# Kernel optimization log

Hardware: AMD Instinct MI355X
Metric: run time of the kernel (lower is better)

Reference implementation:

```python
import jax, jax.numpy as jnp
import numpy as np

B, N, F_IN, F_OUT, H = 4, 2048, 128, 256, 4
HD = F_OUT // H


def setup_inputs() -> dict:
    key = jax.random.key(0)
    k1, k2, k3, k4, k5 = jax.random.split(key, 5)
    x = jax.random.normal(k1, (B, N, F_IN), dtype=jnp.float32)
    adj = jax.random.randint(k2, (B, N, N), 0, 2, dtype=jnp.int32)
    # xavier-ish scaled params
    W = jax.random.normal(k3, (F_OUT, F_IN), dtype=jnp.float32) * float(np.sqrt(2.0 / (F_IN + F_OUT)))
    a_l = jax.random.normal(k4, (H, HD), dtype=jnp.float32) * float(np.sqrt(2.0 / (H * HD + 1)))
    a_r = jax.random.normal(k5, (H, HD), dtype=jnp.float32) * float(np.sqrt(2.0 / (H * HD + 1)))
    return {"x": x, "adj": adj, "W": W, "a_l": a_l, "a_r": a_r}


def reference(x, adj, W, a_l, a_r):
    Bb, Nn, _ = x.shape
    h = jnp.einsum('bnf,of->bno', x, W).reshape(Bb, Nn, H, HD)   # [B,N,H,HD]
    e_l = jnp.einsum('bnhd,hd->bnh', h, a_l)                      # [B,N,H]
    e_r = jnp.einsum('bnhd,hd->bnh', h, a_r)                      # [B,N,H]
    e = e_l[:, :, None, :] + e_r[:, None, :, :]                   # [B,N(i),N(j),H]
    e = jax.nn.leaky_relu(e, negative_slope=0.2)
    e = jnp.where(adj[..., None] == 0, -jnp.inf, e)
    alpha = jax.nn.softmax(e, axis=2)                             # softmax over neighbors j
    out = jnp.einsum('bijh,bjhd->bihd', alpha, h)                 # [B,N,H,HD]
    return out.reshape(Bb, Nn, F_OUT)
```

## Files before the change

kernel.cpp:

```cpp
#include <hip/hip_runtime.h>
#include <stdint.h>

#define BB 4
#define NN 2048
#define F_IN 128
#define F_OUT 256
#define NH 4
#define HD 64

typedef float f32x4 __attribute__((ext_vector_type(4)));
typedef float f32x2 __attribute__((ext_vector_type(2)));
typedef short s16x8 __attribute__((ext_vector_type(8)));
typedef int i32x4 __attribute__((ext_vector_type(4)));
typedef unsigned long long u64;
typedef unsigned short u16;

#define LOG2E 1.4426950408889634f

__device__ __forceinline__ u16 f32_to_bf16_rtn(float f) {
    union { float f; uint32_t u; } v; v.f = f;
    uint32_t u = v.u;
    u += 0x7fffu + ((u >> 16) & 1u);
    return (u16)(u >> 16);
}

__device__ __forceinline__ float exp2_fast(float x) {
#if __has_builtin(__builtin_amdgcn_exp2f)
    return __builtin_amdgcn_exp2f(x);
#else
    return exp2f(x);
#endif
}

__device__ __forceinline__ int sbfe1(uint32_t v, int k) {
#if __has_builtin(__builtin_amdgcn_sbfe)
    return __builtin_amdgcn_sbfe((int)v, k, 1);
#else
    return ((int32_t)(v << (31 - k))) >> 31;
#endif
}

__global__ __launch_bounds__(256) void k01(
    const int* __restrict__ adj, const float* __restrict__ x,
    const float* __restrict__ W, const float* __restrict__ a_l,
    const float* __restrict__ a_r, u64* __restrict__ abits,
    u16* __restrict__ hB, float* __restrict__ el, f32x2* __restrict__ er12)
{
    const int t = threadIdx.x;

    __shared__ __align__(16) float xs[16][F_IN];
    __shared__ __align__(16) float redl[4 * 64 * 20];
    __shared__ __align__(16) float redr[4 * 64 * 20];

    if (blockIdx.x >= 512) {
        const int wid = ((blockIdx.x - 512) << 2) | (t >> 6);
        const int lane = t & 63;
        const int* rowp = adj + (size_t)wid * NN;
        u64 mym = 0;
#pragma unroll 8
        for (int jt = 0; jt < 32; ++jt) {
            int v = rowp[jt * 64 + lane];
            u64 m = __ballot(v != 0);
            if (lane == jt) mym = m;
        }
        if (lane < 32) abits[(size_t)wid * 32 + lane] = mym;
        return;
    }

    const int b = blockIdx.x >> 7;
    const int n0 = (blockIdx.x & 127) * 16;

    {
        const f32x4* src = (const f32x4*)(x + ((size_t)b * NN + n0) * F_IN);
        f32x4* dst = (f32x4*)&xs[0][0];
        dst[t] = src[t];
        dst[t + 256] = src[t + 256];
    }
    __syncthreads();

    float acc[16];
#pragma unroll
    for (int n = 0; n < 16; ++n) acc[n] = 0.f;

    const float* wrow = W + (size_t)t * F_IN;
#pragma unroll 2
    for (int k0 = 0; k0 < F_IN; k0 += 8) {
        f32x4 w0 = *(const f32x4*)(wrow + k0);
        f32x4 w1 = *(const f32x4*)(wrow + k0 + 4);
#pragma unroll
        for (int n = 0; n < 16; ++n) {
            f32x4 xa = *(const f32x4*)&xs[n][k0];
            f32x4 xb = *(const f32x4*)&xs[n][k0 + 4];
            float s = acc[n];
            s = fmaf(xa[0], w0[0], s); s = fmaf(xa[1], w0[1], s);
            s = fmaf(xa[2], w0[2], s); s = fmaf(xa[3], w0[3], s);
            s = fmaf(xb[0], w1[0], s); s = fmaf(xb[1], w1[1], s);
            s = fmaf(xb[2], w1[2], s); s = fmaf(xb[3], w1[3], s);
            acc[n] = s;
        }
    }

    const int w = t >> 6, lane = t & 63;
    const float al = a_l[t];
    const float ar = a_r[t];
    {
        float* rl = &redl[((size_t)w * 64 + lane) * 20];
        float* rr = &redr[((size_t)w * 64 + lane) * 20];
#pragma unroll
        for (int q = 0; q < 4; ++q) {
            f32x4 vl, vr;
#pragma unroll
            for (int e = 0; e < 4; ++e) {
                vl[e] = acc[q * 4 + e] * al;
                vr[e] = acc[q * 4 + e] * ar;
            }
            *(f32x4*)(rl + q * 4) = vl;
            *(f32x4*)(rr + q * 4) = vr;
        }
    }
    __syncthreads();
    {
        const int n_ = lane & 15, og = lane >> 4;
        float sl = 0.f, sr = 0.f;
#pragma unroll
        for (int oo = 0; oo < 16; ++oo) {
            const int o = og + 4 * oo;
            sl += redl[((size_t)w * 64 + o) * 20 + n_];
            sr += redr[((size_t)w * 64 + o) * 20 + n_];
        }
        sl += __shfl_xor(sl, 16, 64); sl += __shfl_xor(sl, 32, 64);
        sr += __shfl_xor(sr, 16, 64); sr += __shfl_xor(sr, 32, 64);
        if (lane < 16) {
            el[((size_t)b * NH + w) * NN + n0 + lane] = sl * LOG2E;
            float sre = sr * LOG2E;
            f32x2 v2; v2[0] = exp2_fast(sre); v2[1] = exp2_fast(0.2f * sre);
            er12[((size_t)b * NH + w) * NN + n0 + lane] = v2;
        }
    }

    const int dcol = t & 15, cb = (t >> 4) & 3;
    const int jt32 = n0 >> 5;
    const int lb = dcol + ((n0 >> 3) & 2) * 16;
    u16* hb = hB + ((((size_t)b * 64 + jt32) * 4 + w) * 4 + cb) * 512 + (size_t)lb * 8;
    s16x8 pk0, pk1;
#pragma unroll
    for (int n = 0; n < 8; ++n) pk0[n] = (short)f32_to_bf16_rtn(acc[n]);
#pragma unroll
    for (int n = 0; n < 8; ++n) pk1[n] = (short)f32_to_bf16_rtn(acc[n + 8]);
    *(s16x8*)hb         = pk0;
    *(s16x8*)(hb + 128) = pk1;
}

__global__ __launch_bounds__(256, 3) void k2_attn(
    const uint32_t* __restrict__ abits32, const u16* __restrict__ hB,
    const float* __restrict__ el, const f32x2* __restrict__ er12,
    float* __restrict__ out)
{
    const int t = threadIdx.x;
    const int jq = t >> 6, l = t & 63;
    int bid = blockIdx.x;
    bid = (bid & 7) * 128 + (bid >> 3);
    const int b = bid >> 8;
    const int w = (bid >> 6) & 3;
    const int i0 = (bid & 63) * 32;
    const int r = l & 15;
    const int kb = l >> 4;
    const int ks = kb * 8;
    const int irow0 = i0 + r, irow1 = irow0 + 16;

    const u16* hbp = hB + ((((size_t)b * 64 + jq * 16) * 4 + w) * 4) * 512 + (size_t)l * 8;
    const f32x2* erp = er12 + ((size_t)b * NH + w) * NN + jq * 512 + ks;
    const i32x4* m0p4 = (const i32x4*)(abits32 + ((size_t)b * NN + irow0) * 64 + jq * 16);
    const i32x4* m1p4 = (const i32x4*)(abits32 + ((size_t)b * NN + irow1) * 64 + jq * 16);

    const float eli0 = el[((size_t)b * NH + w) * NN + irow0];
    const float eli1 = el[((size_t)b * NH + w) * NN + irow1];
    const float E1i0 = exp2_fast(eli0), E2i0 = exp2_fast(0.2f * eli0);
    const float E1i1 = exp2_fast(eli1), E2i1 = exp2_fast(0.2f * eli1);

    f32x4 a00 = {0.f,0.f,0.f,0.f}, a01 = a00, a02 = a00, a03 = a00, as0 = a00;
    f32x4 a10 = a00, a11 = a00, a12 = a00, a13 = a00, as1 = a00;
    s16x8 ones;
#pragma unroll
    for (int k = 0; k < 8; ++k) ones[k] = (short)0x3F80;

    i32x4 mg0c = m0p4[0], mg1c = m1p4[0];
    s16x8 b0c = *(const s16x8*)(hbp + 0 * 512);
    s16x8 b1c = *(const s16x8*)(hbp + 1 * 512);
    s16x8 b2c = *(const s16x8*)(hbp + 2 * 512);
    s16x8 b3c = *(const s16x8*)(hbp + 3 * 512);
    f32x4 v0c = *(const f32x4*)(erp);
    f32x4 v1c = *(const f32x4*)(erp + 2);
    f32x4 v2c = *(const f32x4*)(erp + 4);
    f32x4 v3c = *(const f32x4*)(erp + 6);
    __builtin_amdgcn_sched_barrier(0);

#define MFMA_BF16 __builtin_amdgcn_mfma_f32_16x16x32_bf16
#define BODY(IT, S, PF)                                                       \
    {                                                                         \
        s16x8 b0n, b1n, b2n, b3n;                                             \
        f32x4 v0n, v1n, v2n, v3n;                                             \
        if (PF) {                        \
            const u16* hp_ = hbp + (size_t)((IT) + 1) * 8192;                 \
            b0n = *(const s16x8*)(hp_ + 0 * 512);                             \
            b1n = *(const s16x8*)(hp_ + 1 * 512);                             \
            b2n = *(const s16x8*)(hp_ + 2 * 512);                             \
            b3n = *(const s16x8*)(hp_ + 3 * 512);                             \
            const f32x2* ep_ = erp + ((IT) + 1) * 32;                         \
            v0n = *(const f32x4*)(ep_);                                       \
            v1n = *(const f32x4*)(ep_ + 2);                                   \
            v2n = *(const f32x4*)(ep_ + 4);                                   \
            v3n = *(const f32x4*)(ep_ + 6);                                   \
        }                                                                     \
        __builtin_amdgcn_sched_barrier(0);                                    \
        uint32_t w2a = ((uint32_t)mg0c[S]) >> ks;                             \
        uint32_t w2b = ((uint32_t)mg1c[S]) >> ks;                             \
        uint32_t pua[8], pub[8];                                              \
        _Pragma("unroll")                                                     \
        for (int k = 0; k < 8; ++k) {                                         \
            f32x4 vv = (k < 2) ? v0c : ((k < 4) ? v1c : ((k < 6) ? v2c : v3c)); \
            float ej1 = vv[(k & 1) * 2];                                      \
            float ej2 = vv[(k & 1) * 2 + 1];                                  \
            float t0 = E1i0 * ej1, m0 = E2i0 * ej2;                           \
            float t1 = E1i1 * ej1, m1 = E2i1 * ej2;                           \
            float p0 = (t0 >= 1.0f) ? t0 : m0;                                \
            float p1 = (t1 >= 1.0f) ? t1 : m1;                                \
            union { float f; uint32_t u; } c0, c1; c0.f = p0; c1.f = p1;      \
            pua[k] = c0.u & (uint32_t)sbfe1(w2a, k);                          \
            pub[k] = c1.u & (uint32_t)sbfe1(w2b, k);                          \
        }                                                                     \
        union { s16x8 v; uint32_t u[4]; } afa, afb;                           \
        afa.u[0] = __builtin_amdgcn_perm(pua[1], pua[0], 0x07060302);         \
        afa.u[1] = __builtin_amdgcn_perm(pua[3], pua[2], 0x07060302);         \
        afa.u[2] = __builtin_amdgcn_perm(pua[5], pua[4], 0x07060302);         \
        afa.u[3] = __builtin_amdgcn_perm(pua[7], pua[6], 0x07060302);         \
        afb.u[0] = __builtin_amdgcn_perm(pub[1], pub[0], 0x07060302);         \
        afb.u[1] = __builtin_amdgcn_perm(pub[3], pub[2], 0x07060302);         \
        afb.u[2] = __builtin_amdgcn_perm(pub[5], pub[4], 0x07060302);         \
        afb.u[3] = __builtin_amdgcn_perm(pub[7], pub[6], 0x07060302);         \
        a00 = MFMA_BF16(afa.v, b0c, a00, 0, 0, 0);                            \
        a01 = MFMA_BF16(afa.v, b1c, a01, 0, 0, 0);                            \
        a02 = MFMA_BF16(afa.v, b2c, a02, 0, 0, 0);                            \
        a03 = MFMA_BF16(afa.v, b3c, a03, 0, 0, 0);                            \
        as0 = MFMA_BF16(afa.v, ones, as0, 0, 0, 0);                           \
        a10 = MFMA_BF16(afb.v, b0c, a10, 0, 0, 0);                            \
        a11 = MFMA_BF16(afb.v, b1c, a11, 0, 0, 0);                            \
        a12 = MFMA_BF16(afb.v, b2c, a12, 0, 0, 0);                            \
        a13 = MFMA_BF16(afb.v, b3c, a13, 0, 0, 0);                            \
        as1 = MFMA_BF16(afb.v, ones, as1, 0, 0, 0);                           \
        if (PF) { b0c = b0n; b1c = b1n; b2c = b2n; b3c = b3n;                 \
                  v0c = v0n; v1c = v1n; v2c = v2n; v3c = v3n; }               \
    }

    for (int g = 0; g < 3; ++g) {
        i32x4 mg0n = m0p4[g + 1];
        i32x4 mg1n = m1p4[g + 1];
        __builtin_amdgcn_sched_barrier(0);
#pragma unroll
        for (int s = 0; s < 4; ++s) {
            const int it = g * 4 + s;
            BODY(it, s, 1);
        }
        mg0c = mg0n; mg1c = mg1n;
    }
#pragma unroll
    for (int s = 0; s < 4; ++s) {
        const int it = 12 + s;
        if (s < 3) { BODY(it, s, 1); } else { BODY(it, s, 0); }
    }

    __shared__ __align__(16) float racc[3 * 64 * 44];
    if (jq > 0) {
        float* p = &racc[((jq - 1) * 64 + l) * 44];
        *(f32x4*)(p +  0) = a00; *(f32x4*)(p +  4) = a01;
        *(f32x4*)(p +  8) = a02; *(f32x4*)(p + 12) = a03;
        *(f32x4*)(p + 16) = as0;
        *(f32x4*)(p + 20) = a10; *(f32x4*)(p + 24) = a11;
        *(f32x4*)(p + 28) = a12; *(f32x4*)(p + 32) = a13;
        *(f32x4*)(p + 36) = as1;
    }
    __syncthreads();
    if (jq == 0) {
#pragma unroll
        for (int s = 0; s < 3; ++s) {
            const float* p = &racc[(s * 64 + l) * 44];
            a00 += *(const f32x4*)(p +  0); a01 += *(const f32x4*)(p +  4);
            a02 += *(const f32x4*)(p +  8); a03 += *(const f32x4*)(p + 12);
            as0 += *(const f32x4*)(p + 16);
            a10 += *(const f32x4*)(p + 20); a11 += *(const f32x4*)(p + 24);
            a12 += *(const f32x4*)(p + 28); a13 += *(const f32x4*)(p + 32);
            as1 += *(const f32x4*)(p + 36);
        }

        float* op = out + ((size_t)b * NN + i0) * F_OUT + w * HD;
#pragma unroll
        for (int q = 0; q < 4; ++q) {
            const int row0 = kb * 4 + q;
            float inv0 = 1.0f / as0[q];
            op[(size_t)row0 * F_OUT +  0 + r] = a00[q] * inv0;
            op[(size_t)row0 * F_OUT + 16 + r] = a01[q] * inv0;
            op[(size_t)row0 * F_OUT + 32 + r] = a02[q] * inv0;
            op[(size_t)row0 * F_OUT + 48 + r] = a03[q] * inv0;
            const int row1 = 16 + kb * 4 + q;
            float inv1 = 1.0f / as1[q];
            op[(size_t)row1 * F_OUT +  0 + r] = a10[q] * inv1;
            op[(size_t)row1 * F_OUT + 16 + r] = a11[q] * inv1;
            op[(size_t)row1 * F_OUT + 32 + r] = a12[q] * inv1;
            op[(size_t)row1 * F_OUT + 48 + r] = a13[q] * inv1;
        }
    }
}

extern "C" void kernel_launch(void* const* d_in, const int* in_sizes, int n_in,
                              void* d_out, int out_size, void* d_ws, size_t ws_size,
                              hipStream_t stream) {
    const float* x   = (const float*)d_in[0];
    const int*   adj = (const int*)d_in[1];
    const float* W   = (const float*)d_in[2];
    const float* a_l = (const float*)d_in[3];
    const float* a_r = (const float*)d_in[4];
    float* out = (float*)d_out;

    char* ws = (char*)d_ws;
    u16*   hB    = (u16*)ws;
    u64*   abits = (u64*)(ws + (size_t)BB * F_OUT * NN * 2);
    float* el    = (float*)(ws + (size_t)BB * F_OUT * NN * 2 + (size_t)BB * NN * 32 * 8);
    f32x2* er12  = (f32x2*)(el + (size_t)BB * NH * NN);

    k01<<<512 + BB * NN / 4, 256, 0, stream>>>(adj, x, W, a_l, a_r, abits, hB, el, er12);
    k2_attn<<<BB * NH * (NN / 32), 256, 0, stream>>>((const uint32_t*)abits, hB, el, er12, out);
}
```

Measured before the change: 48.01 us.

## Stage er and mask tiles in LDS, raise k2 occupancy, shrink k01 shared memory

In the attention kernel, the per-head er12 vector and the 32-row adjacency bitmask tile are loaded cooperatively into shared memory once per block. The inner loop then reads them from LDS instead of issuing per-iteration global prefetches, which frees registers and allows the launch bound to rise from 3 to 4 blocks per CU. The reduction buffer is aliased onto the same shared memory after an extra barrier. In k01, the two reduction buffers are merged into one that is used twice with added barriers to cut LDS use, and the adjacency bit-packing loop batches eight loads before its ballots. The trade-off is more LDS traffic and extra syncs in exchange for fewer global loads and higher occupancy.

```diff
diff --git a/kernel.cpp b/kernel.cpp
--- a/kernel.cpp
+++ b/kernel.cpp
@@ -49,19 +49,22 @@
     const int t = threadIdx.x;
 
     __shared__ __align__(16) float xs[16][F_IN];
-    __shared__ __align__(16) float redl[4 * 64 * 20];
-    __shared__ __align__(16) float redr[4 * 64 * 20];
+    __shared__ __align__(16) float red[4 * 64 * 20];
 
     if (blockIdx.x >= 512) {
         const int wid = ((blockIdx.x - 512) << 2) | (t >> 6);
         const int lane = t & 63;
         const int* rowp = adj + (size_t)wid * NN;
         u64 mym = 0;
-#pragma unroll 8
-        for (int jt = 0; jt < 32; ++jt) {
-            int v = rowp[jt * 64 + lane];
-            u64 m = __ballot(v != 0);
-            if (lane == jt) mym = m;
+        for (int g = 0; g < 4; ++g) {
+            int v[8];
+#pragma unroll
+            for (int u = 0; u < 8; ++u) v[u] = rowp[(g * 8 + u) * 64 + lane];
+#pragma unroll
+            for (int u = 0; u < 8; ++u) {
+                u64 m = __ballot(v[u] != 0);
+                if (lane == g * 8 + u) mym = m;
+            }
         }
         if (lane < 32) abits[(size_t)wid * 32 + lane] = mym;
         return;
@@ -103,39 +106,52 @@
     const int w = t >> 6, lane = t & 63;
     const float al = a_l[t];
     const float ar = a_r[t];
-    {
-        float* rl = &redl[((size_t)w * 64 + lane) * 20];
-        float* rr = &redr[((size_t)w * 64 + lane) * 20];
+    const int n_ = lane & 15, og = lane >> 4;
+    float sl, sr;
+    {
+        float* rp = &red[((size_t)w * 64 + lane) * 20];
 #pragma unroll
         for (int q = 0; q < 4; ++q) {
-            f32x4 vl, vr;
-#pragma unroll
-            for (int e = 0; e < 4; ++e) {
-                vl[e] = acc[q * 4 + e] * al;
-                vr[e] = acc[q * 4 + e] * ar;
-            }
-            *(f32x4*)(rl + q * 4) = vl;
-            *(f32x4*)(rr + q * 4) = vr;
-        }
-    }
-    __syncthreads();
-    {
-        const int n_ = lane & 15, og = lane >> 4;
-        float sl = 0.f, sr = 0.f;
-#pragma unroll
-        for (int oo = 0; oo < 16; ++oo) {
-            const int o = og + 4 * oo;
-            sl += redl[((size_t)w * 64 + o) * 20 + n_];
-            sr += redr[((size_t)w * 64 + o) * 20 + n_];
-        }
-        sl += __shfl_xor(sl, 16, 64); sl += __shfl_xor(sl, 32, 64);
-        sr += __shfl_xor(sr, 16, 64); sr += __shfl_xor(sr, 32, 64);
-        if (lane < 16) {
-            el[((size_t)b * NH + w) * NN + n0 + lane] = sl * LOG2E;
-            float sre = sr * LOG2E;
-            f32x2 v2; v2[0] = exp2_fast(sre); v2[1] = exp2_fast(0.2f * sre);
-            er12[((size_t)b * NH + w) * NN + n0 + lane] = v2;
-        }
+            f32x4 v;
+#pragma unroll
+            for (int e = 0; e < 4; ++e) v[e] = acc[q * 4 + e] * al;
+            *(f32x4*)(rp + q * 4) = v;
+        }
+    }
+    __syncthreads();
+    {
+        float s = 0.f;
+#pragma unroll
+        for (int oo = 0; oo < 16; ++oo)
+            s += red[((size_t)w * 64 + og + 4 * oo) * 20 + n_];
+        s += __shfl_xor(s, 16, 64); s += __shfl_xor(s, 32, 64);
+        sl = s;
+    }
+    __syncthreads();
+    {
+        float* rp = &red[((size_t)w * 64 + lane) * 20];
+#pragma unroll
+        for (int q = 0; q < 4; ++q) {
+            f32x4 v;
+#pragma unroll
+            for (int e = 0; e < 4; ++e) v[e] = acc[q * 4 + e] * ar;
+            *(f32x4*)(rp + q * 4) = v;
+        }
+    }
+    __syncthreads();
+    {
+        float s = 0.f;
+#pragma unroll
+        for (int oo = 0; oo < 16; ++oo)
+            s += red[((size_t)w * 64 + og + 4 * oo) * 20 + n_];
+        s += __shfl_xor(s, 16, 64); s += __shfl_xor(s, 32, 64);
+        sr = s;
+    }
+    if (lane < 16) {
+        el[((size_t)b * NH + w) * NN + n0 + lane] = sl * LOG2E;
+        float sre = sr * LOG2E;
+        f32x2 v2; v2[0] = exp2_fast(sre); v2[1] = exp2_fast(0.2f * sre);
+        er12[((size_t)b * NH + w) * NN + n0 + lane] = v2;
     }
 
     const int dcol = t & 15, cb = (t >> 4) & 3;
@@ -151,11 +167,18 @@
     *(s16x8*)(hb + 128) = pk1;
 }
 
-__global__ __launch_bounds__(256, 3) void k2_attn(
+#define MSTRIDE 68
+
+__global__ __launch_bounds__(256, 4) void k2_attn(
     const uint32_t* __restrict__ abits32, const u16* __restrict__ hB,
     const float* __restrict__ el, const f32x2* __restrict__ er12,
     float* __restrict__ out)
 {
+    __shared__ __align__(16) char smem[33792];
+    float*    er_lds   = (float*)smem;
+    uint32_t* mask_lds = (uint32_t*)(smem + 16384);
+    float*    racc     = (float*)smem;
+
     const int t = threadIdx.x;
     const int jq = t >> 6, l = t & 63;
     int bid = blockIdx.x;
@@ -168,11 +191,20 @@
     const int ks = kb * 8;
     const int irow0 = i0 + r, irow1 = irow0 + 16;
 
+    {
+        const f32x4* gsrc = (const f32x4*)(er12 + (size_t)(b * NH + w) * NN);
+        f32x4* edst = (f32x4*)er_lds;
+#pragma unroll
+        for (int p = 0; p < 4; ++p) edst[t + p * 256] = gsrc[t + p * 256];
+        const i32x4* msrc = (const i32x4*)(abits32 + ((size_t)b * NN + i0) * 64);
+        i32x4 mv0 = msrc[t * 2];
+        i32x4 mv1 = msrc[t * 2 + 1];
+        const int mrow = t >> 3, mc = (t & 7) * 8;
+        *(i32x4*)&mask_lds[mrow * MSTRIDE + mc]     = mv0;
+        *(i32x4*)&mask_lds[mrow * MSTRIDE + mc + 4] = mv1;
+    }
+
     const u16* hbp = hB + ((((size_t)b * 64 + jq * 16) * 4 + w) * 4) * 512 + (size_t)l * 8;
-    const f32x2* erp = er12 + ((size_t)b * NH + w) * NN + jq * 512 + ks;
-    const i32x4* m0p4 = (const i32x4*)(abits32 + ((size_t)b * NN + irow0) * 64 + jq * 16);
-    const i32x4* m1p4 = (const i32x4*)(abits32 + ((size_t)b * NN + irow1) * 64 + jq * 16);
-
     const float eli0 = el[((size_t)b * NH + w) * NN + irow0];
     const float eli1 = el[((size_t)b * NH + w) * NN + irow1];
     const float E1i0 = exp2_fast(eli0), E2i0 = exp2_fast(0.2f * eli0);
@@ -184,60 +216,53 @@
 #pragma unroll
     for (int k = 0; k < 8; ++k) ones[k] = (short)0x3F80;
 
-    i32x4 mg0c = m0p4[0], mg1c = m1p4[0];
     s16x8 b0c = *(const s16x8*)(hbp + 0 * 512);
     s16x8 b1c = *(const s16x8*)(hbp + 1 * 512);
     s16x8 b2c = *(const s16x8*)(hbp + 2 * 512);
     s16x8 b3c = *(const s16x8*)(hbp + 3 * 512);
-    f32x4 v0c = *(const f32x4*)(erp);
-    f32x4 v1c = *(const f32x4*)(erp + 2);
-    f32x4 v2c = *(const f32x4*)(erp + 4);
-    f32x4 v3c = *(const f32x4*)(erp + 6);
-    __builtin_amdgcn_sched_barrier(0);
+    __syncthreads();
 
 #define MFMA_BF16 __builtin_amdgcn_mfma_f32_16x16x32_bf16
-#define BODY(IT, S, PF)                                                       \
+#define BODY(IT, PF)                                                          \
     {                                                                         \
+        const int itv = (IT);                                                 \
+        const int jb2 = (jq * 512 + itv * 32 + ks) * 2;                       \
+        f32x4 e0 = *(const f32x4*)(er_lds + jb2);                             \
+        f32x4 e1 = *(const f32x4*)(er_lds + jb2 + 4);                         \
+        f32x4 e2 = *(const f32x4*)(er_lds + jb2 + 8);                         \
+        f32x4 e3 = *(const f32x4*)(er_lds + jb2 + 12);                        \
+        uint32_t w2a = mask_lds[r * MSTRIDE + jq * 16 + itv] >> ks;           \
+        uint32_t w2b = mask_lds[(16 + r) * MSTRIDE + jq * 16 + itv] >> ks;    \
         s16x8 b0n, b1n, b2n, b3n;                                             \
-        f32x4 v0n, v1n, v2n, v3n;                                             \
-        if (PF) {                        \
-            const u16* hp_ = hbp + (size_t)((IT) + 1) * 8192;                 \
+        if (PF) {                                                             \
+            const u16* hp_ = hbp + (size_t)(itv + 1) * 8192;                  \
             b0n = *(const s16x8*)(hp_ + 0 * 512);                             \
             b1n = *(const s16x8*)(hp_ + 1 * 512);                             \
             b2n = *(const s16x8*)(hp_ + 2 * 512);                             \
             b3n = *(const s16x8*)(hp_ + 3 * 512);                             \
-            const f32x2* ep_ = erp + ((IT) + 1) * 32;                         \
-            v0n = *(const f32x4*)(ep_);                                       \
-            v1n = *(const f32x4*)(ep_ + 2);                                   \
-            v2n = *(const f32x4*)(ep_ + 4);                                   \
-            v3n = *(const f32x4*)(ep_ + 6);                                   \
         }                                                                     \
         __builtin_amdgcn_sched_barrier(0);                                    \
-        uint32_t w2a = ((uint32_t)mg0c[S]) >> ks;                             \
-        uint32_t w2b = ((uint32_t)mg1c[S]) >> ks;                             \
-        uint32_t pua[8], pub[8];                                              \
+        union { s16x8 v; uint32_t u[4]; } afa, afb;                           \
         _Pragma("unroll")                                                     \
-        for (int k = 0; k < 8; ++k) {                                         \
-            f32x4 vv = (k < 2) ? v0c : ((k < 4) ? v1c : ((k < 6) ? v2c : v3c)); \
-            float ej1 = vv[(k & 1) * 2];                                      \
-            float ej2 = vv[(k & 1) * 2 + 1];                                  \
-            float t0 = E1i0 * ej1, m0 = E2i0 * ej2;                           \
-            float t1 = E1i1 * ej1, m1 = E2i1 * ej2;                           \
-            float p0 = (t0 >= 1.0f) ? t0 : m0;                                \
-            float p1 = (t1 >= 1.0f) ? t1 : m1;                                \
-            union { float f; uint32_t u; } c0, c1; c0.f = p0; c1.f = p1;      \
-            pua[k] = c0.u & (uint32_t)sbfe1(w2a, k);                          \
-            pub[k] = c1.u & (uint32_t)sbfe1(w2b, k);                          \
+        for (int kk = 0; kk < 4; ++kk) {                                      \
+            f32x4 ev = (kk == 0) ? e0 : ((kk == 1) ? e1 : ((kk == 2) ? e2 : e3)); \
+            float t00 = E1i0 * ev[0], m00 = E2i0 * ev[1];                     \
+            float t01 = E1i0 * ev[2], m01 = E2i0 * ev[3];                     \
+            float t10 = E1i1 * ev[0], m10 = E2i1 * ev[1];                     \
+            float t11 = E1i1 * ev[2], m11 = E2i1 * ev[3];                     \
+            float p00 = (t00 >= 1.0f) ? t00 : m00;                            \
+            float p01 = (t01 >= 1.0f) ? t01 : m01;                            \
+            float p10 = (t10 >= 1.0f) ? t10 : m10;                            \
+            float p11 = (t11 >= 1.0f) ? t11 : m11;                            \
+            union { float f; uint32_t u; } c00, c01, c10, c11;                \
+            c00.f = p00; c01.f = p01; c10.f = p10; c11.f = p11;               \
+            uint32_t q00 = c00.u & (uint32_t)sbfe1(w2a, 2 * kk);              \
+            uint32_t q01 = c01.u & (uint32_t)sbfe1(w2a, 2 * kk + 1);          \
+            uint32_t q10 = c10.u & (uint32_t)sbfe1(w2b, 2 * kk);              \
+            uint32_t q11 = c11.u & (uint32_t)sbfe1(w2b, 2 * kk + 1);          \
+            afa.u[kk] = __builtin_amdgcn_perm(q01, q00, 0x07060302);          \
+            afb.u[kk] = __builtin_amdgcn_perm(q11, q10, 0x07060302);          \
         }                                                                     \
-        union { s16x8 v; uint32_t u[4]; } afa, afb;                           \
-        afa.u[0] = __builtin_amdgcn_perm(pua[1], pua[0], 0x07060302);         \
-        afa.u[1] = __builtin_amdgcn_perm(pua[3], pua[2], 0x07060302);         \
-        afa.u[2] = __builtin_amdgcn_perm(pua[5], pua[4], 0x07060302);         \
-        afa.u[3] = __builtin_amdgcn_perm(pua[7], pua[6], 0x07060302);         \
-        afb.u[0] = __builtin_amdgcn_perm(pub[1], pub[0], 0x07060302);         \
-        afb.u[1] = __builtin_amdgcn_perm(pub[3], pub[2], 0x07060302);         \
-        afb.u[2] = __builtin_amdgcn_perm(pub[5], pub[4], 0x07060302);         \
-        afb.u[3] = __builtin_amdgcn_perm(pub[7], pub[6], 0x07060302);         \
         a00 = MFMA_BF16(afa.v, b0c, a00, 0, 0, 0);                            \
         a01 = MFMA_BF16(afa.v, b1c, a01, 0, 0, 0);                            \
         a02 = MFMA_BF16(afa.v, b2c, a02, 0, 0, 0);                            \
@@ -248,28 +273,16 @@
         a12 = MFMA_BF16(afb.v, b2c, a12, 0, 0, 0);                            \
         a13 = MFMA_BF16(afb.v, b3c, a13, 0, 0, 0);                            \
         as1 = MFMA_BF16(afb.v, ones, as1, 0, 0, 0);                           \
-        if (PF) { b0c = b0n; b1c = b1n; b2c = b2n; b3c = b3n;                 \
-                  v0c = v0n; v1c = v1n; v2c = v2n; v3c = v3n; }               \
+        if (PF) { b0c = b0n; b1c = b1n; b2c = b2n; b3c = b3n; }               \
     }
 
     for (int g = 0; g < 3; ++g) {
-        i32x4 mg0n = m0p4[g + 1];
-        i32x4 mg1n = m1p4[g + 1];
-        __builtin_amdgcn_sched_barrier(0);
-#pragma unroll
-        for (int s = 0; s < 4; ++s) {
-            const int it = g * 4 + s;
-            BODY(it, s, 1);
-        }
-        mg0c = mg0n; mg1c = mg1n;
-    }
-#pragma unroll
-    for (int s = 0; s < 4; ++s) {
-        const int it = 12 + s;
-        if (s < 3) { BODY(it, s, 1); } else { BODY(it, s, 0); }
-    }
-
-    __shared__ __align__(16) float racc[3 * 64 * 44];
+#pragma unroll
+        for (int s = 0; s < 4; ++s) BODY(g * 4 + s, 1);
+    }
+    BODY(12, 1); BODY(13, 1); BODY(14, 1); BODY(15, 0);
+
+    __syncthreads();
     if (jq > 0) {
         float* p = &racc[((jq - 1) * 64 + l) * 44];
         *(f32x4*)(p +  0) = a00; *(f32x4*)(p +  4) = a01;
```

New measurement: 49.01 us. 1.02x slower.
